# Performance work log

Hardware: AMD Instinct MI355X
Metric: run time of the kernel (lower is better)

The kernel has to match this reference:

```python
import jax, jax.numpy as jnp
import numpy as np
import math

D = 768; H = 12; DH = D // H; FF = 3072; B = 8; S = 512
D_K_NEIGHBOR = 64.0
EPS = 1e-5

def _linear(x, W, b):
    return x @ W + b

def _layernorm(x, g, b):
    m = jnp.mean(x, axis=-1, keepdims=True)
    v = jnp.var(x, axis=-1, keepdims=True)
    return (x - m) * jax.lax.rsqrt(v + EPS) * g + b

def setup_inputs():
    key = jax.random.key(0)
    ks = jax.random.split(key, 24)
    w = lambda k, shape: (0.02 * jax.random.normal(k, shape)).astype(jnp.float32)
    z = lambda n: jnp.zeros((n,), jnp.float32)
    return {
        'x': jax.random.normal(ks[0], (B, S, D), dtype=jnp.float32),
        'src_padding_mask': jnp.ones((B, S), dtype=bool),
        'prev_affinity_scores_a': jax.random.uniform(ks[1], (B, S - 1), dtype=jnp.float32),
        'Wqn': w(ks[2], (D, D)), 'bqn': z(D),
        'Wkn': w(ks[3], (D, D)), 'bkn': z(D),
        'Wq': w(ks[4], (D, D)), 'bq': z(D),
        'Wk': w(ks[5], (D, D)), 'bk': z(D),
        'Wv': w(ks[6], (D, D)), 'bv': z(D),
        'Wo': w(ks[7], (D, D)), 'bo': z(D),
        'W1': w(ks[8], (D, FF)), 'b1': z(FF),
        'W2': w(ks[9], (FF, D)), 'b2': z(D),
        'g1': jnp.ones((D,), jnp.float32), 'be1': z(D),
        'g2': jnp.ones((D,), jnp.float32), 'be2': z(D),
        'layer_idx': 0,
    }

def _affinity(x, Wqn, bqn, Wkn, bkn, prev_a, layer_idx):
    q = _linear(x, Wqn, bqn)  # [B,S,D]
    k = _linear(x, Wkn, bkn)
    s_fwd = jnp.sum(q[:, :-1] * k[:, 1:], axis=-1) / D_K_NEIGHBOR  # [B,S-1]
    s_bwd = jnp.sum(q[:, 1:] * k[:, :-1], axis=-1) / D_K_NEIGHBOR
    a_hat = (jax.nn.sigmoid(s_fwd) + jax.nn.sigmoid(s_bwd)) * 0.5
    if layer_idx == 0:
        return a_hat
    return prev_a + (1.0 - prev_a) * a_hat

def _mask_C(a):
    # C[b,i,j] = prod_{t=min(i,j)}^{max(i,j)-1} a[b,t]; diag = 1.
    # Log-space prefix sums replace the O(S^2) python loop of the original:
    # L[k] = sum_{t<k} log a[t]; C[i,j] = exp(L[max(i,j)] - L[min(i,j)]).
    L = jnp.concatenate([jnp.zeros((a.shape[0], 1), a.dtype),
                         jnp.cumsum(jnp.log(a), axis=1)], axis=1)  # [B,S]
    ii = jnp.arange(S)
    imin = jnp.minimum(ii[:, None], ii[None, :])
    imax = jnp.maximum(ii[:, None], ii[None, :])
    C = jnp.exp(L[:, imax] - L[:, imin])  # [B,S,S]
    return C[:, None]  # [B,1,S,S]

def reference(x, src_padding_mask, prev_affinity_scores_a, Wqn, bqn, Wkn, bkn,
              Wq, bq, Wk, bk, Wv, bv, Wo, bo, W1, b1, W2, b2, g1, be1, g2, be2,
              layer_idx):
    a = _affinity(x, Wqn, bqn, Wkn, bkn, prev_affinity_scores_a, layer_idx)
    C = _mask_C(a)
    residual = x
    xn = _layernorm(x, g1, be1)
    q = _linear(xn, Wq, bq).reshape(B, S, H, DH).transpose(0, 2, 1, 3)
    k = _linear(xn, Wk, bk).reshape(B, S, H, DH).transpose(0, 2, 1, 3)
    v = _linear(xn, Wv, bv).reshape(B, S, H, DH).transpose(0, 2, 1, 3)
    scores = jnp.einsum('bhqd,bhkd->bhqk', q, k) / math.sqrt(DH)
    scores = jnp.where(src_padding_mask[:, None, None, :], scores, -1e9)
    attn = jax.nn.softmax(scores, axis=-1)
    attn_h = C * attn  # hierarchical masking of attention weights
    ctx = jnp.einsum('bhqk,bhkd->bhqd', attn_h, v)
    ctx = ctx.transpose(0, 2, 1, 3).reshape(B, S, D)
    x1 = residual + _linear(ctx, Wo, bo)
    xn2 = _layernorm(x1, g2, be2)
    ffn = _linear(jax.nn.relu(_linear(xn2, W1, b1)), W2, b2)
    out = x1 + ffn
    return out, a, attn_h
```

## Files before the change

kernel.cpp:

```cpp
#include <hip/hip_runtime.h>
#include <math.h>

#define B_  8
#define S_  512
#define D_  768
#define H_  12
#define DH_ 64
#define FF_ 3072
#define M_  (B_ * S_)

typedef unsigned short u16;
typedef unsigned int   u32;
typedef __bf16  bf16x8 __attribute__((ext_vector_type(8)));
typedef float   f32x4  __attribute__((ext_vector_type(4)));
typedef unsigned short u16x4 __attribute__((ext_vector_type(4)));

__device__ __forceinline__ float b2f(u16 h) {
    union { u32 u; float f; } v; v.u = ((u32)h) << 16; return v.f;
}
__device__ __forceinline__ u16 f2b(float f) {
    union { u32 u; float f; } v; v.f = f;
    u32 u = v.u;
    u32 r = (u + 0x7FFFu + ((u >> 16) & 1u)) >> 16;
    return (u16)r;
}

__device__ __forceinline__ void gload16(const void* g, void* l) {
    __builtin_amdgcn_global_load_lds(
        (const __attribute__((address_space(1))) void*)g,
        (__attribute__((address_space(3))) void*)l, 16, 0, 0);
}

__global__ void cast_f32_bf16(const float* __restrict__ X, u16* __restrict__ Y, int n4) {
    int i4 = (blockIdx.x * 256 + threadIdx.x);
    if (i4 >= n4) return;
    f32x4 v = *(const f32x4*)(X + (size_t)i4 * 4);
    u16x4 o;
    o.x = f2b(v.x); o.y = f2b(v.y); o.z = f2b(v.z); o.w = f2b(v.w);
    *(u16x4*)(Y + (size_t)i4 * 4) = o;
}

__global__ void transpose6(const float* s0, const float* s1, const float* s2,
                           const float* s3, const float* s4, const float* s5,
                           u16* d0, u16* d1, u16* d2, u16* d3, u16* d4, u16* d5)
{
    __shared__ u16 tile[32][33];
    int z = blockIdx.z;
    const float* W = (z == 0) ? s0 : (z == 1) ? s1 : (z == 2) ? s2
                   : (z == 3) ? s3 : (z == 4) ? s4 : s5;
    u16* WT = (z == 0) ? d0 : (z == 1) ? d1 : (z == 2) ? d2
            : (z == 3) ? d3 : (z == 4) ? d4 : d5;
    int c0 = blockIdx.x * 32, r0 = blockIdx.y * 32;
    int tx = threadIdx.x, ty = threadIdx.y;
    #pragma unroll
    for (int j = 0; j < 32; j += 8)
        tile[ty + j][tx] = f2b(W[(size_t)(r0 + ty + j) * D_ + (c0 + tx)]);
    __syncthreads();
    #pragma unroll
    for (int j = 0; j < 32; j += 8)
        WT[(size_t)(c0 + ty + j) * D_ + (r0 + tx)] = tile[tx][ty + j];
}

__global__ void transpose_cast(const float* __restrict__ W, u16* __restrict__ WT,
                               int R, int C) {
    __shared__ u16 tile[32][33];
    int c0 = blockIdx.x * 32;
    int r0 = blockIdx.y * 32;
    int tx = threadIdx.x, ty = threadIdx.y;
    #pragma unroll
    for (int j = 0; j < 32; j += 8)
        tile[ty + j][tx] = f2b(W[(size_t)(r0 + ty + j) * C + (c0 + tx)]);
    __syncthreads();
    #pragma unroll
    for (int j = 0; j < 32; j += 8)
        WT[(size_t)(c0 + ty + j) * R + (r0 + tx)] = tile[tx][ty + j];
}

__global__ void bias_concat(const float* bqn, const float* bkn, const float* bq,
                            const float* bk, const float* bv,
                            float* bias_nk, float* bias_qkv)
{
    int i = blockIdx.x * 256 + threadIdx.x;
    if (i < 768)       bias_nk[i] = bqn[i];
    else if (i < 1536) bias_nk[i] = bkn[i - 768];
    else if (i < 2304) bias_qkv[i - 1536] = bq[i - 1536];
    else if (i < 3072) bias_qkv[i - 1536] = bk[i - 2304];
    else if (i < 3840) bias_qkv[i - 1536] = bv[i - 3072];
}

__launch_bounds__(256)
__global__ void gemm_mfma(const u16* __restrict__ A, const u16* __restrict__ BT,
                          const float* __restrict__ bias, const float* __restrict__ res,
                          u16* __restrict__ Cb, float* __restrict__ Cf,
                          int N, int K, int klen, int relu, int split)
{
    __shared__ __align__(16) u16 As[128 * 64];
    __shared__ __align__(16) u16 Bs[128 * 64];
    int tid = threadIdx.x;
    int wave = tid >> 6, lane = tid & 63;
    int m0 = blockIdx.y * 128, n0 = blockIdx.x * 128;
    int kbeg = blockIdx.z * klen;
    int wm = (wave >> 1) * 64, wn = (wave & 1) * 64;
    int r16 = lane & 15, kq = lane >> 4;
    f32x4 acc[4][4] = {};
    for (int k0 = 0; k0 < klen; k0 += 64) {
        #pragma unroll
        for (int i = 0; i < 4; ++i) {
            int cid = i * 256 + tid;
            int row = cid >> 3, phys = cid & 7, logc = phys ^ (row & 7);
            gload16(&A [(size_t)(m0 + row) * K + kbeg + k0 + logc * 8], &As[cid * 8]);
            gload16(&BT[(size_t)(n0 + row) * K + kbeg + k0 + logc * 8], &Bs[cid * 8]);
        }
        __syncthreads();
        #pragma unroll
        for (int ks = 0; ks < 2; ++ks) {
            bf16x8 af[4], bfr[4];
            #pragma unroll
            for (int i = 0; i < 4; ++i) {
                int row = wm + i * 16 + r16;
                af[i] = *(const bf16x8*)&As[row * 64 + (((ks * 4 + kq) ^ (row & 7)) * 8)];
            }
            #pragma unroll
            for (int j = 0; j < 4; ++j) {
                int row = wn + j * 16 + r16;
                bfr[j] = *(const bf16x8*)&Bs[row * 64 + (((ks * 4 + kq) ^ (row & 7)) * 8)];
            }
            #pragma unroll
            for (int i = 0; i < 4; ++i)
                #pragma unroll
                for (int j = 0; j < 4; ++j)
                    acc[i][j] = __builtin_amdgcn_mfma_f32_16x16x32_bf16(
                        af[i], bfr[j], acc[i][j], 0, 0, 0);
        }
        __syncthreads();
    }
    if (split) {
        float* Pf = Cf + (size_t)blockIdx.z * M_ * N;
        #pragma unroll
        for (int i = 0; i < 4; ++i) {
            int rg = m0 + wm + i * 16 + kq * 4;
            #pragma unroll
            for (int j = 0; j < 4; ++j) {
                int cg = n0 + wn + j * 16 + r16;
                #pragma unroll
                for (int r = 0; r < 4; ++r)
                    Pf[(size_t)(rg + r) * N + cg] = acc[i][j][r];
            }
        }
        return;
    }
    #pragma unroll
    for (int i = 0; i < 4; ++i) {
        int rg = m0 + wm + i * 16 + kq * 4;
        #pragma unroll
        for (int j = 0; j < 4; ++j) {
            int cg = n0 + wn + j * 16 + r16;
            float bc = bias[cg];
            #pragma unroll
            for (int r = 0; r < 4; ++r) {
                float v = acc[i][j][r] + bc;
                if (relu) v = fmaxf(v, 0.f);
                size_t off = (size_t)(rg + r) * N + cg;
                if (res) v += res[off];
                if (Cb) Cb[off] = f2b(v);
                if (Cf) Cf[off] = v;
            }
        }
    }
}

__global__ void reduce_k(const float* __restrict__ parts, int KS,
                         const float* __restrict__ res, const float* __restrict__ bias,
                         float* __restrict__ out, int N, int n4)
{
    int i4 = blockIdx.x * 256 + threadIdx.x;
    if (i4 >= n4) return;
    size_t base = (size_t)i4 * 4;
    int col = (int)(base % N);
    f32x4 acc = *(const f32x4*)(res + base);
    f32x4 bv = *(const f32x4*)(bias + col);
    acc.x += bv.x; acc.y += bv.y; acc.z += bv.z; acc.w += bv.w;
    const size_t MN = (size_t)M_ * N;
    for (int s = 0; s < KS; ++s) {
        f32x4 p = *(const f32x4*)(parts + s * MN + base);
        acc.x += p.x; acc.y += p.y; acc.z += p.z; acc.w += p.w;
    }
    *(f32x4*)(out + base) = acc;
}

__global__ void affinity_k(const u16* __restrict__ nk,
                           const float* __restrict__ prev, const int* __restrict__ lidx,
                           float* __restrict__ a_out)
{
    const int ST = 2 * D_;
    int gid  = blockIdx.x * 4 + (threadIdx.x >> 6);
    int lane = threadIdx.x & 63;
    if (gid >= B_ * (S_ - 1)) return;
    int b = gid / (S_ - 1), i = gid % (S_ - 1);
    const u16* q0 = nk + (size_t)(b * S_ + i)     * ST;
    const u16* q1 = nk + (size_t)(b * S_ + i + 1) * ST;
    const u16* k0 = q0 + D_;
    const u16* k1 = q1 + D_;
    float sf = 0.f, sb = 0.f;
    for (int d = lane; d < D_; d += 64) {
        sf += b2f(q0[d]) * b2f(k1[d]);
        sb += b2f(q1[d]) * b2f(k0[d]);
    }
    #pragma unroll
    for (int off = 32; off > 0; off >>= 1) {
        sf += __shfl_xor(sf, off);
        sb += __shfl_xor(sb, off);
    }
    if (lane == 0) {
        sf *= (1.f / 64.f); sb *= (1.f / 64.f);
        float ah = 0.5f * (1.f / (1.f + expf(-sf)) + 1.f / (1.f + expf(-sb)));
        float a = ah;
        if (lidx[0] != 0) { float p = prev[gid]; a = p + (1.f - p) * ah; }
        a_out[gid] = a;
    }
}

__global__ void cumsum_k(const float* __restrict__ a_f, float* __restrict__ L) {
    int b = blockIdx.x;
    int lane = threadIdx.x;
    float lg[8]; float s = 0.f;
    #pragma unroll
    for (int r = 0; r < 8; ++r) {
        int t = lane * 8 + r;
        lg[r] = (t < S_ - 1) ? logf(fmaxf(a_f[b * (S_ - 1) + t], 1e-35f)) : 0.f;
        s += lg[r];
    }
    float incl = s;
    #pragma unroll
    for (int off = 1; off < 64; off <<= 1) {
        float n = __shfl_up(incl, off);
        if (lane >= off) incl += n;
    }
    float run = incl - s;
    #pragma unroll
    for (int r = 0; r < 8; ++r) {
        L[b * S_ + lane * 8 + r] = run;
        run += lg[r];
    }
}

__global__ void layernorm_k(const float* __restrict__ X, const float* __restrict__ g,
                            const float* __restrict__ be, u16* __restrict__ Y)
{
    int row  = blockIdx.x * 4 + (threadIdx.x >> 6);
    int lane = threadIdx.x & 63;
    const float* xr = X + (size_t)row * D_;
    float xs[12], s = 0.f, sq = 0.f;
    #pragma unroll
    for (int t = 0; t < 12; ++t) {
        float v = xr[lane + t * 64];
        xs[t] = v; s += v; sq += v * v;
    }
    #pragma unroll
    for (int off = 32; off > 0; off >>= 1) {
        s  += __shfl_xor(s, off);
        sq += __shfl_xor(sq, off);
    }
    float m  = s  * (1.f / (float)D_);
    float var = sq * (1.f / (float)D_) - m * m;
    float rs = rsqrtf(var + 1e-5f);
    u16* yr = Y + (size_t)row * D_;
    #pragma unroll
    for (int t = 0; t < 12; ++t) {
        int d = lane + t * 64;
        yr[d] = f2b((xs[t] - m) * rs * g[d] + be[d]);
    }
}

__global__ void vt_transpose(const u16* __restrict__ QKV, u16* __restrict__ Vt) {
    const int ST = 3 * D_;
    __shared__ u16 tile[32][33];
    int bh = blockIdx.z; int b = bh / H_, h = bh % H_;
    int j0 = blockIdx.x * 32;
    int d0 = blockIdx.y * 32;
    int tx = threadIdx.x, ty = threadIdx.y;
    #pragma unroll
    for (int jj = 0; jj < 32; jj += 8)
        tile[ty + jj][tx] = QKV[(size_t)(b * S_ + j0 + ty + jj) * ST + 2 * D_ + h * DH_ + d0 + tx];
    __syncthreads();
    #pragma unroll
    for (int jj = 0; jj < 32; jj += 8)
        Vt[((size_t)bh * DH_ + d0 + ty + jj) * S_ + (j0 + tx)] = tile[tx][ty + jj];
}

__launch_bounds__(256, 2)
__global__ void qk_softmax_c(const u16* __restrict__ QKV, const float* __restrict__ L,
                             float* __restrict__ Attn)
{
    const int ST = 3 * D_;
    __shared__ __align__(16) u16 Ks[S_ * 64];
    __shared__ __align__(16) u16 Qs[64 * 64];
    __shared__ float Lsh[S_];
    int bh = blockIdx.y; int b = bh / H_, h = bh % H_;
    int q0 = blockIdx.x * 64;
    int tid = threadIdx.x;
    int wave = tid >> 6, lane = tid & 63;
    int r16 = lane & 15, kq = lane >> 4;
    #pragma unroll
    for (int i = 0; i < 2; ++i) {
        int cid = i * 256 + tid;
        int row = cid >> 3, logc = (cid & 7) ^ (row & 7);
        gload16(&QKV[(size_t)(b * S_ + q0 + row) * ST + h * DH_ + logc * 8], &Qs[cid * 8]);
    }
    #pragma unroll
    for (int i = 0; i < 16; ++i) {
        int cid = i * 256 + tid;
        int row = cid >> 3, logc = (cid & 7) ^ (row & 7);
        gload16(&QKV[(size_t)(b * S_ + row) * ST + D_ + h * DH_ + logc * 8], &Ks[cid * 8]);
    }
    for (int j = tid; j < S_; j += 256) Lsh[j] = L[b * S_ + j];
    __syncthreads();
    int arow = wave * 16 + r16;
    bf16x8 a0 = *(const bf16x8*)&Qs[arow * 64 + (((kq)     ^ (arow & 7)) * 8)];
    bf16x8 a1 = *(const bf16x8*)&Qs[arow * 64 + (((4 + kq) ^ (arow & 7)) * 8)];
    f32x4 acc[32];
    #pragma unroll
    for (int jt = 0; jt < 32; ++jt) {
        int brow = jt * 16 + r16;
        bf16x8 b0 = *(const bf16x8*)&Ks[brow * 64 + (((kq)     ^ (brow & 7)) * 8)];
        bf16x8 b1 = *(const bf16x8*)&Ks[brow * 64 + (((4 + kq) ^ (brow & 7)) * 8)];
        f32x4 z = {0.f, 0.f, 0.f, 0.f};
        z = __builtin_amdgcn_mfma_f32_16x16x32_bf16(a0, b0, z, 0, 0, 0);
        acc[jt] = __builtin_amdgcn_mfma_f32_16x16x32_bf16(a1, b1, z, 0, 0, 0);
    }
    float mxv[4] = {-1e30f, -1e30f, -1e30f, -1e30f};
    #pragma unroll
    for (int jt = 0; jt < 32; ++jt)
        #pragma unroll
        for (int r = 0; r < 4; ++r)
            mxv[r] = fmaxf(mxv[r], acc[jt][r] * 0.125f);
    #pragma unroll
    for (int mk = 1; mk <= 8; mk <<= 1)
        #pragma unroll
        for (int r = 0; r < 4; ++r)
            mxv[r] = fmaxf(mxv[r], __shfl_xor(mxv[r], mk));
    float sum[4] = {0.f, 0.f, 0.f, 0.f};
    #pragma unroll
    for (int jt = 0; jt < 32; ++jt)
        #pragma unroll
        for (int r = 0; r < 4; ++r) {
            float e = expf(acc[jt][r] * 0.125f - mxv[r]);
            acc[jt][r] = e; sum[r] += e;
        }
    #pragma unroll
    for (int mk = 1; mk <= 8; mk <<= 1)
        #pragma unroll
        for (int r = 0; r < 4; ++r)
            sum[r] += __shfl_xor(sum[r], mk);
    float inv[4], Lq[4]; int qrow[4];
    #pragma unroll
    for (int r = 0; r < 4; ++r) {
        inv[r] = 1.f / sum[r];
        qrow[r] = q0 + wave * 16 + kq * 4 + r;
        Lq[r] = Lsh[qrow[r]];
    }
    size_t obase = (size_t)bh * S_ * S_;
    #pragma unroll
    for (int jt = 0; jt < 32; ++jt) {
        int j = jt * 16 + r16;
        float Lj = Lsh[j];
        #pragma unroll
        for (int r = 0; r < 4; ++r) {
            float d = (j >= qrow[r]) ? (Lj - Lq[r]) : (Lq[r] - Lj);
            float pv = acc[jt][r] * inv[r] * expf(fminf(d, 0.f));
            Attn[obase + (size_t)qrow[r] * S_ + j] = pv;
        }
    }
}

__launch_bounds__(256)
__global__ void av_mfma(const float* __restrict__ Attn, const u16* __restrict__ Vt,
                        u16* __restrict__ ctx)
{
    const int LP = 136;
    __shared__ __align__(16) u16 Ps[128 * LP];
    __shared__ __align__(16) u16 Vs[64 * LP];
    int bh = blockIdx.y; int b = bh / H_, h = bh % H_;
    int q0 = blockIdx.x * 128;
    int tid = threadIdx.x;
    int wave = tid >> 6, lane = tid & 63;
    int wq = wave * 32;
    int r16 = lane & 15, kq = lane >> 4;
    f32x4 acc[2][4] = {};
    size_t abase = ((size_t)bh * S_ + q0) * S_;
    const u16* vtb = Vt + (size_t)bh * DH_ * S_;
    int prow = tid >> 1, pcb = (tid & 1) * 64;
    int vrow = tid >> 2, vcb = (tid & 3) * 32;
    for (int jc = 0; jc < S_; jc += 128) {
        {
            const float* pg = Attn + abase + (size_t)prow * S_ + jc + pcb;
            u16* pl = &Ps[prow * LP + pcb];
            #pragma unroll
            for (int c = 0; c < 8; ++c) {
                f32x4 a = *(const f32x4*)(pg + c * 8);
                f32x4 bvv = *(const f32x4*)(pg + c * 8 + 4);
                u16 tmp[8];
                tmp[0]=f2b(a.x); tmp[1]=f2b(a.y); tmp[2]=f2b(a.z); tmp[3]=f2b(a.w);
                tmp[4]=f2b(bvv.x); tmp[5]=f2b(bvv.y); tmp[6]=f2b(bvv.z); tmp[7]=f2b(bvv.w);
                *(u16x4*)(pl + c * 8)     = *(u16x4*)&tmp[0];
                *(u16x4*)(pl + c * 8 + 4) = *(u16x4*)&tmp[4];
            }
        }
        {
            const u16* vg = vtb + (size_t)vrow * S_ + jc + vcb;
            u16* vl = &Vs[vrow * LP + vcb];
            #pragma unroll
            for (int c = 0; c < 4; ++c)
                *(bf16x8*)(vl + c * 8) = *(const bf16x8*)(vg + c * 8);
        }
        __syncthreads();
        #pragma unroll
        for (int ks = 0; ks < 4; ++ks) {
            bf16x8 af[2], bfr[4];
            #pragma unroll
            for (int i = 0; i < 2; ++i)
                af[i] = *(const bf16x8*)&Ps[(wq + i * 16 + r16) * LP + ks * 32 + kq * 8];
            #pragma unroll
            for (int n = 0; n < 4; ++n)
                bfr[n] = *(const bf16x8*)&Vs[(n * 16 + r16) * LP + ks * 32 + kq * 8];
            #pragma unroll
            for (int i = 0; i < 2; ++i)
                #pragma unroll
                for (int n = 0; n < 4; ++n)
                    acc[i][n] = __builtin_amdgcn_mfma_f32_16x16x32_bf16(
                        af[i], bfr[n], acc[i][n], 0, 0, 0);
        }
        __syncthreads();
    }
    #pragma unroll
    for (int i = 0; i < 2; ++i) {
        int qg = q0 + wq + i * 16 + kq * 4;
        #pragma unroll
        for (int n = 0; n < 4; ++n) {
            int d = n * 16 + r16;
            #pragma unroll
            for (int r = 0; r < 4; ++r)
                ctx[(size_t)(b * S_ + qg + r) * D_ + h * DH_ + d] = f2b(acc[i][n][r]);
        }
    }
}

extern "C" void kernel_launch(void* const* d_in, const int* in_sizes, int n_in,
                              void* d_out, int out_size, void* d_ws, size_t ws_size,
                              hipStream_t stream) {
    const float* x    = (const float*)d_in[0];
    const float* prev = (const float*)d_in[2];
    const float* Wqn = (const float*)d_in[3];  const float* bqn = (const float*)d_in[4];
    const float* Wkn = (const float*)d_in[5];  const float* bkn = (const float*)d_in[6];
    const float* Wq  = (const float*)d_in[7];  const float* bq  = (const float*)d_in[8];
    const float* Wk  = (const float*)d_in[9];  const float* bk  = (const float*)d_in[10];
    const float* Wv  = (const float*)d_in[11]; const float* bv  = (const float*)d_in[12];
    const float* Wo  = (const float*)d_in[13]; const float* bo  = (const float*)d_in[14];
    const float* W1  = (const float*)d_in[15]; const float* b1  = (const float*)d_in[16];
    const float* W2  = (const float*)d_in[17]; const float* b2  = (const float*)d_in[18];
    const float* g1  = (const float*)d_in[19]; const float* be1 = (const float*)d_in[20];
    const float* g2  = (const float*)d_in[21]; const float* be2 = (const float*)d_in[22];
    const int* lidx = (const int*)d_in[23];

    char* ws = (char*)d_ws;
    size_t off = 0;
    auto alloc = [&](size_t bytes) -> void* {
        void* p = ws + off; off += (bytes + 255) & ~(size_t)255; return p;
    };
    const size_t DDe = (size_t)D_ * D_;
    u16* WT_nk  = (u16*)alloc(2 * DDe * 2);
    u16* WT_qkv = (u16*)alloc(3 * DDe * 2);
    u16* WT_o   = (u16*)alloc(DDe * 2);
    u16* W1T    = (u16*)alloc((size_t)FF_ * D_ * 2);
    u16* W2T    = (u16*)alloc((size_t)FF_ * D_ * 2);
    float* bias_nk  = (float*)alloc(2 * D_ * 4);
    float* bias_qkv = (float*)alloc(3 * D_ * 4);
    u16* xb    = (u16*)alloc((size_t)M_ * D_ * 2);
    u16* nk_b  = (u16*)alloc((size_t)M_ * 2 * D_ * 2);
    u16* qkv_b = (u16*)alloc((size_t)M_ * 3 * D_ * 2);
    float* L_f = (float*)alloc((size_t)B_ * S_ * 4);
    u16* xn_b  = (u16*)alloc((size_t)M_ * D_ * 2);
    u16* ctx_b = (u16*)alloc((size_t)M_ * D_ * 2);
    float* x1_f = (float*)alloc((size_t)M_ * D_ * 4);
    float* parts = (float*)alloc((size_t)4 * M_ * D_ * 4);
    u16* h_b = nk_b;
    u16* xn2_b = xn_b;
    u16* Vt = xb;

    float* out0     = (float*)d_out;
    float* out_a    = out0 + (size_t)M_ * D_;
    float* out_attn = out_a + (size_t)B_ * (S_ - 1);

    dim3 tb(32, 8);
    cast_f32_bf16<<<(M_ * D_ / 4 + 255) / 256, 256, 0, stream>>>(x, xb, M_ * D_ / 4);
    transpose6<<<dim3(D_/32, D_/32, 6), tb, 0, stream>>>(
        Wqn, Wkn, Wq, Wk, Wv, Wo,
        WT_nk, WT_nk + DDe, WT_qkv, WT_qkv + DDe, WT_qkv + 2 * DDe, WT_o);
    transpose_cast<<<dim3(FF_/32, D_/32), tb, 0, stream>>>(W1, W1T, D_, FF_);
    transpose_cast<<<dim3(D_/32, FF_/32), tb, 0, stream>>>(W2, W2T, FF_, D_);
    bias_concat<<<15, 256, 0, stream>>>(bqn, bkn, bq, bk, bv, bias_nk, bias_qkv);

    gemm_mfma<<<dim3(2*D_/128, M_/128), 256, 0, stream>>>(
        xb, WT_nk, bias_nk, nullptr, nk_b, nullptr, 2*D_, D_, D_, 0, 0);
    affinity_k<<<(B_ * (S_ - 1) + 3) / 4, 256, 0, stream>>>(nk_b, prev, lidx, out_a);
    cumsum_k<<<B_, 64, 0, stream>>>(out_a, L_f);

    layernorm_k<<<M_ / 4, 256, 0, stream>>>(x, g1, be1, xn_b);
    gemm_mfma<<<dim3(3*D_/128, M_/128), 256, 0, stream>>>(
        xn_b, WT_qkv, bias_qkv, nullptr, qkv_b, nullptr, 3*D_, D_, D_, 0, 0);

    vt_transpose<<<dim3(S_/32, DH_/32, B_*H_), tb, 0, stream>>>(qkv_b, Vt);
    qk_softmax_c<<<dim3(S_/64, B_*H_), 256, 0, stream>>>(qkv_b, L_f, out_attn);
    av_mfma<<<dim3(S_/128, B_*H_), 256, 0, stream>>>(out_attn, Vt, ctx_b);

    gemm_mfma<<<dim3(D_/128, M_/128, 2), 256, 0, stream>>>(
        ctx_b, WT_o, nullptr, nullptr, nullptr, parts, D_, D_, D_/2, 0, 1);
    reduce_k<<<(M_ * D_ / 4 + 255) / 256, 256, 0, stream>>>(
        parts, 2, x, bo, x1_f, D_, M_ * D_ / 4);
    layernorm_k<<<M_ / 4, 256, 0, stream>>>(x1_f, g2, be2, xn2_b);
    gemm_mfma<<<dim3(FF_/128, M_/128), 256, 0, stream>>>(
        xn2_b, W1T, b1, nullptr, h_b, nullptr, FF_, D_, D_, 1, 0);
    gemm_mfma<<<dim3(D_/128, M_/128, 4), 256, 0, stream>>>(
        h_b, W2T, nullptr, nullptr, nullptr, parts, D_, FF_, FF_/4, 0, 1);
    reduce_k<<<(M_ * D_ / 4 + 255) / 256, 256, 0, stream>>>(
        parts, 4, x1_f, b2, out0, D_, M_ * D_ / 4);
}
```

Measured before the change: 460.8 us.

## Fuse softmax with PV matmul, and fuse layernorm with cast and reduce

```diff
diff --git a/kernel.cpp b/kernel.cpp
--- a/kernel.cpp
+++ b/kernel.cpp
@@ -14,6 +14,7 @@
 typedef __bf16  bf16x8 __attribute__((ext_vector_type(8)));
 typedef float   f32x4  __attribute__((ext_vector_type(4)));
 typedef unsigned short u16x4 __attribute__((ext_vector_type(4)));
+typedef unsigned int   u32x2 __attribute__((ext_vector_type(2)));
 
 __device__ __forceinline__ float b2f(u16 h) {
     union { u32 u; float f; } v; v.u = ((u32)h) << 16; return v.f;
@@ -29,15 +30,6 @@
     __builtin_amdgcn_global_load_lds(
         (const __attribute__((address_space(1))) void*)g,
         (__attribute__((address_space(3))) void*)l, 16, 0, 0);
-}
-
-__global__ void cast_f32_bf16(const float* __restrict__ X, u16* __restrict__ Y, int n4) {
-    int i4 = (blockIdx.x * 256 + threadIdx.x);
-    if (i4 >= n4) return;
-    f32x4 v = *(const f32x4*)(X + (size_t)i4 * 4);
-    u16x4 o;
-    o.x = f2b(v.x); o.y = f2b(v.y); o.z = f2b(v.z); o.w = f2b(v.w);
-    *(u16x4*)(Y + (size_t)i4 * 4) = o;
 }
 
 __global__ void transpose6(const float* s0, const float* s1, const float* s2,
@@ -186,6 +178,100 @@
         acc.x += p.x; acc.y += p.y; acc.z += p.z; acc.w += p.w;
     }
     *(f32x4*)(out + base) = acc;
+}
+
+__global__ void reduce_ln_k(const float* __restrict__ parts, int KS,
+                            const float* __restrict__ res, const float* __restrict__ bias,
+                            const float* __restrict__ g, const float* __restrict__ be,
+                            float* __restrict__ Xout, u16* __restrict__ Y)
+{
+    int row  = blockIdx.x * 4 + (threadIdx.x >> 6);
+    int lane = threadIdx.x & 63;
+    size_t rb = (size_t)row * D_;
+    f32x4 xv[3];
+    float s = 0.f, sq = 0.f;
+    #pragma unroll
+    for (int t = 0; t < 3; ++t) {
+        int d = lane * 4 + t * 256;
+        f32x4 a  = *(const f32x4*)(res + rb + d);
+        f32x4 bv = *(const f32x4*)(bias + d);
+        a.x += bv.x; a.y += bv.y; a.z += bv.z; a.w += bv.w;
+        for (int ss = 0; ss < KS; ++ss) {
+            f32x4 p = *(const f32x4*)(parts + (size_t)ss * M_ * D_ + rb + d);
+            a.x += p.x; a.y += p.y; a.z += p.z; a.w += p.w;
+        }
+        *(f32x4*)(Xout + rb + d) = a;
+        xv[t] = a;
+        #pragma unroll
+        for (int e = 0; e < 4; ++e) { float v = a[e]; s += v; sq += v * v; }
+    }
+    #pragma unroll
+    for (int off = 32; off > 0; off >>= 1) {
+        s  += __shfl_xor(s, off);
+        sq += __shfl_xor(sq, off);
+    }
+    float m  = s * (1.f / (float)D_);
+    float var = sq * (1.f / (float)D_) - m * m;
+    float rs = rsqrtf(var + 1e-5f);
+    u16* yr = Y + rb;
+    #pragma unroll
+    for (int t = 0; t < 3; ++t) {
+        int d = lane * 4 + t * 256;
+        f32x4 gv = *(const f32x4*)(g + d);
+        f32x4 bv = *(const f32x4*)(be + d);
+        u16x4 o;
+        #pragma unroll
+        for (int e = 0; e < 4; ++e)
+            o[e] = f2b((xv[t][e] - m) * rs * gv[e] + bv[e]);
+        *(u16x4*)(yr + d) = o;
+    }
+}
+
+__global__ void ln_cast_k(const float* __restrict__ X, const float* __restrict__ g,
+                          const float* __restrict__ be, u16* __restrict__ Y,
+                          u16* __restrict__ Ycast)
+{
+    int row  = blockIdx.x * 4 + (threadIdx.x >> 6);
+    int lane = threadIdx.x & 63;
+    const float* xr = X + (size_t)row * D_;
+    f32x4 xv[3];
+    float s = 0.f, sq = 0.f;
+    #pragma unroll
+    for (int t = 0; t < 3; ++t) {
+        xv[t] = *(const f32x4*)(xr + lane * 4 + t * 256);
+        #pragma unroll
+        for (int e = 0; e < 4; ++e) { float v = xv[t][e]; s += v; sq += v * v; }
+    }
+    if (Ycast) {
+        u16* yc = Ycast + (size_t)row * D_;
+        #pragma unroll
+        for (int t = 0; t < 3; ++t) {
+            u16x4 o;
+            #pragma unroll
+            for (int e = 0; e < 4; ++e) o[e] = f2b(xv[t][e]);
+            *(u16x4*)(yc + lane * 4 + t * 256) = o;
+        }
+    }
+    #pragma unroll
+    for (int off = 32; off > 0; off >>= 1) {
+        s  += __shfl_xor(s, off);
+        sq += __shfl_xor(sq, off);
+    }
+    float m  = s * (1.f / (float)D_);
+    float var = sq * (1.f / (float)D_) - m * m;
+    float rs = rsqrtf(var + 1e-5f);
+    u16* yr = Y + (size_t)row * D_;
+    #pragma unroll
+    for (int t = 0; t < 3; ++t) {
+        int d = lane * 4 + t * 256;
+        f32x4 gv = *(const f32x4*)(g + d);
+        f32x4 bv = *(const f32x4*)(be + d);
+        u16x4 o;
+        #pragma unroll
+        for (int e = 0; e < 4; ++e)
+            o[e] = f2b((xv[t][e] - m) * rs * gv[e] + bv[e]);
+        *(u16x4*)(yr + d) = o;
+    }
 }
 
 __global__ void affinity_k(const u16* __restrict__ nk,
@@ -244,34 +330,6 @@
     }
 }
 
-__global__ void layernorm_k(const float* __restrict__ X, const float* __restrict__ g,
-                            const float* __restrict__ be, u16* __restrict__ Y)
-{
-    int row  = blockIdx.x * 4 + (threadIdx.x >> 6);
-    int lane = threadIdx.x & 63;
-    const float* xr = X + (size_t)row * D_;
-    float xs[12], s = 0.f, sq = 0.f;
-    #pragma unroll
-    for (int t = 0; t < 12; ++t) {
-        float v = xr[lane + t * 64];
-        xs[t] = v; s += v; sq += v * v;
-    }
-    #pragma unroll
-    for (int off = 32; off > 0; off >>= 1) {
-        s  += __shfl_xor(s, off);
-        sq += __shfl_xor(sq, off);
-    }
-    float m  = s  * (1.f / (float)D_);
-    float var = sq * (1.f / (float)D_) - m * m;
-    float rs = rsqrtf(var + 1e-5f);
-    u16* yr = Y + (size_t)row * D_;
-    #pragma unroll
-    for (int t = 0; t < 12; ++t) {
-        int d = lane + t * 64;
-        yr[d] = f2b((xs[t] - m) * rs * g[d] + be[d]);
-    }
-}
-
 __global__ void vt_transpose(const u16* __restrict__ QKV, u16* __restrict__ Vt) {
     const int ST = 3 * D_;
     __shared__ u16 tile[32][33];
@@ -288,9 +346,10 @@
         Vt[((size_t)bh * DH_ + d0 + ty + jj) * S_ + (j0 + tx)] = tile[tx][ty + jj];
 }
 
-__launch_bounds__(256, 2)
-__global__ void qk_softmax_c(const u16* __restrict__ QKV, const float* __restrict__ L,
-                             float* __restrict__ Attn)
+__launch_bounds__(256)
+__global__ void attn_fused(const u16* __restrict__ QKV, const u16* __restrict__ Vt,
+                           const float* __restrict__ L,
+                           float* __restrict__ Attn, u16* __restrict__ ctx)
 {
     const int ST = 3 * D_;
     __shared__ __align__(16) u16 Ks[S_ * 64];
@@ -301,6 +360,7 @@
     int tid = threadIdx.x;
     int wave = tid >> 6, lane = tid & 63;
     int r16 = lane & 15, kq = lane >> 4;
+
     #pragma unroll
     for (int i = 0; i < 2; ++i) {
         int cid = i * 256 + tid;
@@ -315,6 +375,7 @@
     }
     for (int j = tid; j < S_; j += 256) Lsh[j] = L[b * S_ + j];
     __syncthreads();
+
     int arow = wave * 16 + r16;
     bf16x8 a0 = *(const bf16x8*)&Qs[arow * 64 + (((kq)     ^ (arow & 7)) * 8)];
     bf16x8 a1 = *(const bf16x8*)&Qs[arow * 64 + (((4 + kq) ^ (arow & 7)) * 8)];
@@ -325,123 +386,83 @@
         bf16x8 b0 = *(const bf16x8*)&Ks[brow * 64 + (((kq)     ^ (brow & 7)) * 8)];
         bf16x8 b1 = *(const bf16x8*)&Ks[brow * 64 + (((4 + kq) ^ (brow & 7)) * 8)];
         f32x4 z = {0.f, 0.f, 0.f, 0.f};
-        z = __builtin_amdgcn_mfma_f32_16x16x32_bf16(a0, b0, z, 0, 0, 0);
-        acc[jt] = __builtin_amdgcn_mfma_f32_16x16x32_bf16(a1, b1, z, 0, 0, 0);
-    }
-    float mxv[4] = {-1e30f, -1e30f, -1e30f, -1e30f};
+        z = __builtin_amdgcn_mfma_f32_16x16x32_bf16(b0, a0, z, 0, 0, 0);
+        acc[jt] = __builtin_amdgcn_mfma_f32_16x16x32_bf16(b1, a1, z, 0, 0, 0);
+    }
+    __syncthreads();
+
+    const u16* vtb = Vt + (size_t)bh * DH_ * S_;
+    #pragma unroll
+    for (int i = 0; i < 16; ++i) {
+        int cid = i * 256 + tid;
+        int d = cid >> 6, p = cid & 63, l = p ^ (d & 7);
+        gload16(&vtb[(size_t)d * S_ + l * 8], &Ks[cid * 8]);
+    }
+
+    float mx = -1e30f;
     #pragma unroll
     for (int jt = 0; jt < 32; ++jt)
         #pragma unroll
         for (int r = 0; r < 4; ++r)
-            mxv[r] = fmaxf(mxv[r], acc[jt][r] * 0.125f);
-    #pragma unroll
-    for (int mk = 1; mk <= 8; mk <<= 1)
+            mx = fmaxf(mx, acc[jt][r] * 0.125f);
+    mx = fmaxf(mx, __shfl_xor(mx, 16));
+    mx = fmaxf(mx, __shfl_xor(mx, 32));
+    float sum = 0.f;
+    #pragma unroll
+    for (int jt = 0; jt < 32; ++jt)
+        #pragma unroll
+        for (int r = 0; r < 4; ++r) {
+            float e = expf(acc[jt][r] * 0.125f - mx);
+            acc[jt][r] = e; sum += e;
+        }
+    sum += __shfl_xor(sum, 16);
+    sum += __shfl_xor(sum, 32);
+    float inv = 1.f / sum;
+    int qg = q0 + wave * 16 + r16;
+    float Lq = Lsh[qg];
+    __syncthreads();
+
+    u16* Pt = &Qs[wave * 1024];
+    size_t obase = (size_t)bh * S_ * S_ + (size_t)qg * S_;
+    f32x4 accpv[4] = {};
+    for (int c = 0; c < 8; ++c) {
+        #pragma unroll
+        for (int jt4 = 0; jt4 < 4; ++jt4) {
+            int jt = c * 4 + jt4;
+            int j0c = jt * 16 + kq * 4;
+            f32x4 Ljv = *(const f32x4*)&Lsh[j0c];
+            f32x4 pv;
+            #pragma unroll
+            for (int r = 0; r < 4; ++r) {
+                int j = j0c + r;
+                float dr = (j >= qg) ? (Ljv[r] - Lq) : (Lq - Ljv[r]);
+                pv[r] = acc[jt][r] * inv * expf(fminf(dr, 0.f));
+            }
+            *(f32x4*)&Attn[obase + j0c] = pv;
+            u32 lo = (u32)f2b(pv[0]) | ((u32)f2b(pv[1]) << 16);
+            u32 hi = (u32)f2b(pv[2]) | ((u32)f2b(pv[3]) << 16);
+            int jloc = jt4 * 16 + kq * 4;
+            u32x2 pk; pk.x = lo; pk.y = hi;
+            *(u32x2*)&Pt[r16 * 64 + (jloc ^ ((r16 & 7) << 3))] = pk;
+        }
+        #pragma unroll
+        for (int ks = 0; ks < 2; ++ks) {
+            bf16x8 ap = *(const bf16x8*)&Pt[r16 * 64 + ((ks * 32 + kq * 8) ^ ((r16 & 7) << 3))];
+            #pragma unroll
+            for (int n = 0; n < 4; ++n) {
+                int d = n * 16 + r16;
+                bf16x8 bv = *(const bf16x8*)&Ks[d * 512 + ((c * 64 + ks * 32 + kq * 8) ^ ((d & 7) << 3))];
+                accpv[n] = __builtin_amdgcn_mfma_f32_16x16x32_bf16(ap, bv, accpv[n], 0, 0, 0);
+            }
+        }
+    }
+    int qq = q0 + wave * 16 + kq * 4;
+    #pragma unroll
+    for (int n = 0; n < 4; ++n) {
+        int d = n * 16 + r16;
         #pragma unroll
         for (int r = 0; r < 4; ++r)
-            mxv[r] = fmaxf(mxv[r], __shfl_xor(mxv[r], mk));
-    float sum[4] = {0.f, 0.f, 0.f, 0.f};
-    #pragma unroll
-    for (int jt = 0; jt < 32; ++jt)
-        #pragma unroll
-        for (int r = 0; r < 4; ++r) {
-            float e = expf(acc[jt][r] * 0.125f - mxv[r]);
-            acc[jt][r] = e; sum[r] += e;
-        }
-    #pragma unroll
-    for (int mk = 1; mk <= 8; mk <<= 1)
-        #pragma unroll
-        for (int r = 0; r < 4; ++r)
-            sum[r] += __shfl_xor(sum[r], mk);
-    float inv[4], Lq[4]; int qrow[4];
-    #pragma unroll
-    for (int r = 0; r < 4; ++r) {
-        inv[r] = 1.f / sum[r];
-        qrow[r] = q0 + wave * 16 + kq * 4 + r;
-        Lq[r] = Lsh[qrow[r]];
-    }
-    size_t obase = (size_t)bh * S_ * S_;
-    #pragma unroll
-    for (int jt = 0; jt < 32; ++jt) {
-        int j = jt * 16 + r16;
-        float Lj = Lsh[j];
-        #pragma unroll
-        for (int r = 0; r < 4; ++r) {
-            float d = (j >= qrow[r]) ? (Lj - Lq[r]) : (Lq[r] - Lj);
-            float pv = acc[jt][r] * inv[r] * expf(fminf(d, 0.f));
-            Attn[obase + (size_t)qrow[r] * S_ + j] = pv;
-        }
-    }
-}
-
-__launch_bounds__(256)
-__global__ void av_mfma(const float* __restrict__ Attn, const u16* __restrict__ Vt,
-                        u16* __restrict__ ctx)
-{
-    const int LP = 136;
-    __shared__ __align__(16) u16 Ps[128 * LP];
-    __shared__ __align__(16) u16 Vs[64 * LP];
-    int bh = blockIdx.y; int b = bh / H_, h = bh % H_;
-    int q0 = blockIdx.x * 128;
-    int tid = threadIdx.x;
-    int wave = tid >> 6, lane = tid & 63;
-    int wq = wave * 32;
-    int r16 = lane & 15, kq = lane >> 4;
-    f32x4 acc[2][4] = {};
-    size_t abase = ((size_t)bh * S_ + q0) * S_;
-    const u16* vtb = Vt + (size_t)bh * DH_ * S_;
-    int prow = tid >> 1, pcb = (tid & 1) * 64;
-    int vrow = tid >> 2, vcb = (tid & 3) * 32;
-    for (int jc = 0; jc < S_; jc += 128) {
-        {
-            const float* pg = Attn + abase + (size_t)prow * S_ + jc + pcb;
-            u16* pl = &Ps[prow * LP + pcb];
-            #pragma unroll
-            for (int c = 0; c < 8; ++c) {
-                f32x4 a = *(const f32x4*)(pg + c * 8);
-                f32x4 bvv = *(const f32x4*)(pg + c * 8 + 4);
-                u16 tmp[8];
-                tmp[0]=f2b(a.x); tmp[1]=f2b(a.y); tmp[2]=f2b(a.z); tmp[3]=f2b(a.w);
-                tmp[4]=f2b(bvv.x); tmp[5]=f2b(bvv.y); tmp[6]=f2b(bvv.z); tmp[7]=f2b(bvv.w);
-                *(u16x4*)(pl + c * 8)     = *(u16x4*)&tmp[0];
-                *(u16x4*)(pl + c * 8 + 4) = *(u16x4*)&tmp[4];
-            }
-        }
-        {
-            const u16* vg = vtb + (size_t)vrow * S_ + jc + vcb;
-            u16* vl = &Vs[vrow * LP + vcb];
-            #pragma unroll
-            for (int c = 0; c < 4; ++c)
-                *(bf16x8*)(vl + c * 8) = *(const bf16x8*)(vg + c * 8);
-        }
-        __syncthreads();
-        #pragma unroll
-        for (int ks = 0; ks < 4; ++ks) {
-            bf16x8 af[2], bfr[4];
-            #pragma unroll
-            for (int i = 0; i < 2; ++i)
-                af[i] = *(const bf16x8*)&Ps[(wq + i * 16 + r16) * LP + ks * 32 + kq * 8];
-            #pragma unroll
-            for (int n = 0; n < 4; ++n)
-                bfr[n] = *(const bf16x8*)&Vs[(n * 16 + r16) * LP + ks * 32 + kq * 8];
-            #pragma unroll
-            for (int i = 0; i < 2; ++i)
-                #pragma unroll
-                for (int n = 0; n < 4; ++n)
-                    acc[i][n] = __builtin_amdgcn_mfma_f32_16x16x32_bf16(
-                        af[i], bfr[n], acc[i][n], 0, 0, 0);
-        }
-        __syncthreads();
-    }
-    #pragma unroll
-    for (int i = 0; i < 2; ++i) {
-        int qg = q0 + wq + i * 16 + kq * 4;
-        #pragma unroll
-        for (int n = 0; n < 4; ++n) {
-            int d = n * 16 + r16;
-            #pragma unroll
-            for (int r = 0; r < 4; ++r)
-                ctx[(size_t)(b * S_ + qg + r) * D_ + h * DH_ + d] = f2b(acc[i][n][r]);
-        }
+            ctx[(size_t)(b * S_ + qq + r) * D_ + h * DH_ + d] = f2b(accpv[n][r]);
     }
 }
 
@@ -492,7 +513,7 @@
     float* out_attn = out_a + (size_t)B_ * (S_ - 1);
 
     dim3 tb(32, 8);
-    cast_f32_bf16<<<(M_ * D_ / 4 + 255) / 256, 256, 0, stream>>>(x, xb, M_ * D_ / 4);
+    ln_cast_k<<<M_ / 4, 256, 0, stream>>>(x, g1, be1, xn_b, xb);
     transpose6<<<dim3(D_/32, D_/32, 6), tb, 0, stream>>>(
         Wqn, Wkn, Wq, Wk, Wv, Wo,
         WT_nk, WT_nk + DDe, WT_qkv, WT_qkv + DDe, WT_qkv + 2 * DDe, WT_o);
@@ -505,19 +526,15 @@
     affinity_k<<<(B_ * (S_ - 1) + 3) / 4, 256, 0, stream>>>(nk_b, prev, lidx, out_a);
     cumsum_k<<<B_, 64, 0, stream>>>(out_a, L_f);
 
-    layernorm_k<<<M_ / 4, 256, 0, stream>>>(x, g1, be1, xn_b);
     gemm_mfma<<<dim3(3*D_/128, M_/128), 256, 0, stream>>>(
         xn_b, WT_qkv, bias_qkv, nullptr, qkv_b, nullptr, 3*D_, D_, D_, 0, 0);
 
     vt_transpose<<<dim3(S_/32, DH_/32, B_*H_), tb, 0, stream>>>(qkv_b, Vt);
-    qk_softmax_c<<<dim3(S_/64, B_*H_), 256, 0, stream>>>(qkv_b, L_f, out_attn);
-    av_mfma<<<dim3(S_/128, B_*H_), 256, 0, stream>>>(out_attn, Vt, ctx_b);
+    attn_fused<<<dim3(S_/64, B_*H_), 256, 0, stream>>>(qkv_b, Vt, L_f, out_attn, ctx_b);
 
     gemm_mfma<<<dim3(D_/128, M_/128, 2), 256, 0, stream>>>(
         ctx_b, WT_o, nullptr, nullptr, nullptr, parts, D_, D_, D_/2, 0, 1);
-    reduce_k<<<(M_ * D_ / 4 + 255) / 256, 256, 0, stream>>>(
-        parts, 2, x, bo, x1_f, D_, M_ * D_ / 4);
-    layernorm_k<<<M_ / 4, 256, 0, stream>>>(x1_f, g2, be2, xn2_b);
+    reduce_ln_k<<<M_ / 4, 256, 0, stream>>>(parts, 2, x, bo, g2, be2, x1_f, xn2_b);
     gemm_mfma<<<dim3(FF_/128, M_/128), 256, 0, stream>>>(
         xn2_b, W1T, b1, nullptr, h_b, nullptr, FF_, D_, D_, 1, 0);
     gemm_mfma<<<dim3(D_/128, M_/128, 4), 256, 0, stream>>>(
```

Result: no change. 454.3 us (-1.4%).
